# Kernel tuning notes

Hardware: AMD Instinct MI355X
Metric: run time of the kernel (lower is better)

The kernel has to match this reference:

```python
import jax, jax.numpy as jnp
import numpy as np

H = 12  # num_heads (ViT-B)


def setup_inputs() -> dict:
    key = jax.random.key(0)
    ks = jax.random.split(key, 16)
    B, N, C = 128, 197, 768
    eff, hd = H // 2, C // H
    d = {
        'x':  jax.random.normal(ks[0], (B, N, C), jnp.float32),
        'Wq': jax.random.normal(ks[1], (C, C), jnp.float32) * 0.02,
        'bq': jax.random.normal(ks[2], (C,), jnp.float32) * 0.02,
        'Wk': jax.random.normal(ks[3], (C, C), jnp.float32) * 0.02,
        'bk': jax.random.normal(ks[4], (C,), jnp.float32) * 0.02,
        'Wv': jax.random.normal(ks[5], (C, C), jnp.float32) * 0.02,
        'bv': jax.random.normal(ks[6], (C,), jnp.float32) * 0.02,
        'Wp': jax.random.normal(ks[7], (C, C), jnp.float32) * 0.02,
        'bp': jax.random.normal(ks[8], (C,), jnp.float32) * 0.02,
        'lq1': jax.random.normal(ks[9],  (eff, 1, hd), jnp.float32) * 0.02,
        'lk1': jax.random.normal(ks[10], (eff, 1, hd), jnp.float32) * 0.02,
        'lq2': jax.random.normal(ks[11], (eff, 1, hd), jnp.float32) * 0.02,
        'lk2': jax.random.normal(ks[12], (eff, 1, hd), jnp.float32) * 0.02,
        'num_heads': 12,
        'lambda_init': jnp.float32(0.8),
    }
    return d


def reference(x, Wq, bq, Wk, bk, Wv, bv, Wp, bp, lq1, lk1, lq2, lk2, num_heads, lambda_init):
    B, N, C = x.shape
    hd = C // num_heads
    scale = hd ** -0.5

    def heads(y):  # [B,N,C] -> [B,H,N,hd]
        return y.reshape(B, N, num_heads, hd).transpose(0, 2, 1, 3)

    q = heads(x @ Wq.T + bq)
    k = heads(x @ Wk.T + bk)
    v = heads(x @ Wv.T + bv)
    eff = num_heads // 2
    q1, q2 = q[:, :eff], q[:, eff:]
    k1, k2 = k[:, :eff], k[:, eff:]
    v1, v2 = v[:, :eff], v[:, eff:]

    l1 = jnp.exp(jnp.minimum((lq1 * lk1).sum((-1, -2)), 5.0))  # [eff]
    l2 = jnp.exp(jnp.minimum((lq2 * lk2).sum((-1, -2)), 5.0))
    lv = (l1 - l2 + lambda_init).mean()  # scalar

    def attn(qh, kh, vh):  # [B,eff,N,hd]
        s = jnp.einsum('bhnd,bhmd->bhnm', qh, kh) * scale
        a = jax.nn.softmax(s, axis=-1)
        o = jnp.einsum('bhnm,bhmd->bhnd', a, vh)
        return o.transpose(0, 2, 1, 3).reshape(B, N, C // 2)

    x1 = attn(q1, k1, v1)
    x2 = attn(q2, k2, v2)
    out = jnp.concatenate([x1 - lv * x2, x2], axis=-1)
    return out @ Wp.T + bp
```

## Files before the change

### kernel.cpp

```cpp
#include <hip/hip_runtime.h>
#include <hip/hip_bf16.h>
#include <stdint.h>


typedef __attribute__((ext_vector_type(4))) float f32x4;
typedef __attribute__((ext_vector_type(8))) short s16x8;
typedef __attribute__((ext_vector_type(8))) __bf16 bf16x8;

typedef const __attribute__((address_space(1))) void* gptr_t;
typedef __attribute__((address_space(3))) void* lptr_t;

__device__ __forceinline__ f32x4 mfma16(s16x8 a, s16x8 b, f32x4 c) {
  return __builtin_amdgcn_mfma_f32_16x16x32_bf16(
      __builtin_bit_cast(bf16x8, a), __builtin_bit_cast(bf16x8, b), c, 0, 0, 0);
}

__device__ __forceinline__ short f2bf(float f) {
  unsigned u = __float_as_uint(f);
  u += 0x7fffu + ((u >> 16) & 1u);
  return (short)(u >> 16);
}
__device__ __forceinline__ float bf2f(short s) {
  return __uint_as_float(((unsigned)(unsigned short)s) << 16);
}

__device__ __forceinline__ void gload_lds16(const void* g, void* l) {
  __builtin_amdgcn_global_load_lds((gptr_t)g, (lptr_t)l, 16, 0, 0);
}

__global__ void cvt_f32_to_bf16(const float* __restrict__ src,
                                short* __restrict__ dst, long n8) {
  long i = (long)blockIdx.x * blockDim.x + threadIdx.x;
  const long stride = (long)gridDim.x * blockDim.x;
  for (; i < n8; i += stride) {
    const float4 a = ((const float4*)src)[2 * i];
    const float4 b = ((const float4*)src)[2 * i + 1];
    s16x8 o;
    o[0] = f2bf(a.x); o[1] = f2bf(a.y); o[2] = f2bf(a.z); o[3] = f2bf(a.w);
    o[4] = f2bf(b.x); o[5] = f2bf(b.y); o[6] = f2bf(b.z); o[7] = f2bf(b.w);
    ((s16x8*)dst)[i] = o;
  }
}

__global__ void lv_kernel(const float* __restrict__ lq1, const float* __restrict__ lk1,
                          const float* __restrict__ lq2, const float* __restrict__ lk2,
                          const float* __restrict__ lambda_init, float* __restrict__ out) {
  const int l = threadIdx.x;
  float v = 0.f;
  if (l < 6) {
    float d1 = 0.f, d2 = 0.f;
    for (int j = 0; j < 64; ++j) {
      d1 += lq1[l * 64 + j] * lk1[l * 64 + j];
      d2 += lq2[l * 64 + j] * lk2[l * 64 + j];
    }
    v = expf(fminf(d1, 5.f)) - expf(fminf(d2, 5.f));
  }
  v += __shfl_xor(v, 1, 64);
  v += __shfl_xor(v, 2, 64);
  v += __shfl_xor(v, 4, 64);
  if (l == 0) out[0] = v * (1.f / 6.f) + lambda_init[0];
}

__global__ void cvt_wp_prime(const float* __restrict__ Wp,
                             const float* __restrict__ lvp,
                             short* __restrict__ dst) {
  const int idx = blockIdx.x * blockDim.x + threadIdx.x;
  if (idx >= 73728) return;
  const float lv = *lvp;
  const int ic = idx % 96;
  const float4 a = ((const float4*)Wp)[2 * idx];
  const float4 b = ((const float4*)Wp)[2 * idx + 1];
  float v[8] = {a.x, a.y, a.z, a.w, b.x, b.y, b.z, b.w};
  if (ic >= 48) {
    const float4 a2 = ((const float4*)Wp)[2 * idx - 96];
    const float4 b2 = ((const float4*)Wp)[2 * idx - 95];
    v[0] -= lv * a2.x; v[1] -= lv * a2.y; v[2] -= lv * a2.z; v[3] -= lv * a2.w;
    v[4] -= lv * b2.x; v[5] -= lv * b2.y; v[6] -= lv * b2.z; v[7] -= lv * b2.w;
  }
  s16x8 o;
#pragma unroll
  for (int j = 0; j < 8; ++j) o[j] = f2bf(v[j]);
  ((s16x8*)dst)[idx] = o;
}

template <int OUT_BF16>
__global__ __launch_bounds__(256) void gemm_bt(const short* __restrict__ A, int lda,
                                               const short* __restrict__ B,
                                               const float* __restrict__ bias,
                                               void* __restrict__ C,
                                               int M, int N, int K) {
  const int nbx = N >> 7;
  const int nwg = gridDim.x;
  const int qq = nwg >> 3, rr = nwg & 7;
  const int xcd = blockIdx.x & 7, pos = blockIdx.x >> 3;
  const int wg = (xcd < rr ? xcd * (qq + 1) : rr * (qq + 1) + (xcd - rr) * qq) + pos;
  const int bx = wg % nbx;
  const int by = wg / nbx;
  const long m0 = (long)by << 7;
  const int n0 = bx << 7;
  __shared__ short Asm[128 * 64];
  __shared__ short Bsm[128 * 64];
  const int tid = threadIdx.x;
  const int lane = tid & 63;
  const int w = tid >> 6;
  const int wr = w >> 1, wc = w & 1;
  const int r16 = lane & 15, g = lane >> 4;
  f32x4 acc[4][4];
#pragma unroll
  for (int i = 0; i < 4; ++i)
#pragma unroll
    for (int j = 0; j < 4; ++j) acc[i][j] = f32x4{0.f, 0.f, 0.f, 0.f};

  const int nkt = K >> 6;
  for (int kt = 0; kt < nkt; ++kt) {
    __syncthreads();
#pragma unroll
    for (int i = 0; i < 4; ++i) {
      const int c = i * 256 + tid;
      const int row = c >> 3;
      const int lc = (c & 7) ^ (row & 7);
      gload_lds16(A + (m0 + row) * lda + (long)kt * 64 + lc * 8,
                  Asm + i * 2048 + w * 512);
      gload_lds16(B + (long)(n0 + row) * K + (long)kt * 64 + lc * 8,
                  Bsm + i * 2048 + w * 512);
    }
    asm volatile("s_waitcnt vmcnt(0)" ::: "memory");
    __syncthreads();
#pragma unroll
    for (int kk = 0; kk < 2; ++kk) {
      s16x8 av[4], bvv[4];
#pragma unroll
      for (int f = 0; f < 4; ++f) {
        const int ar = wr * 64 + f * 16 + r16;
        av[f] = *(const s16x8*)(Asm + ar * 64 + ((((kk << 2) + g) ^ (ar & 7)) << 3));
        const int br = wc * 64 + f * 16 + r16;
        bvv[f] = *(const s16x8*)(Bsm + br * 64 + ((((kk << 2) + g) ^ (br & 7)) << 3));
      }
#pragma unroll
      for (int fm = 0; fm < 4; ++fm)
#pragma unroll
        for (int fn = 0; fn < 4; ++fn)
          acc[fm][fn] = mfma16(av[fm], bvv[fn], acc[fm][fn]);
    }
  }
#pragma unroll
  for (int fm = 0; fm < 4; ++fm)
#pragma unroll
    for (int fn = 0; fn < 4; ++fn) {
      const int col = n0 + wc * 64 + fn * 16 + r16;
      const float bb = bias[col];
#pragma unroll
      for (int r = 0; r < 4; ++r) {
        const long row = m0 + wr * 64 + fm * 16 + g * 4 + r;
        const float v = acc[fm][fn][r] + bb;
        if (OUT_BF16) ((short*)C)[row * (long)N + col] = f2bf(v);
        else          ((float*)C)[row * (long)N + col] = v;
      }
    }
}

__global__ __launch_bounds__(512, 4) void attn_kernel(short* QKV) {
  const int b = blockIdx.x / 12;
  const int h = blockIdx.x % 12;
  __shared__ short Ksm[208 * 72];
  __shared__ short Vsm[64 * 232];
  __shared__ short Psm[8][2][512];
  const int tid = threadIdx.x;
  const long base = (long)b * 197 * 2304;

  for (int c = tid; c < 208 * 8; c += 512) {
    const int key = c >> 3, dch = c & 7;
    s16x8 val = {};
    if (key < 197)
      val = *(const s16x8*)(QKV + base + (long)key * 2304 + 768 + h * 64 + dch * 8);
    *(s16x8*)(Ksm + key * 72 + dch * 8) = val;
  }
  for (int c = tid; c < 224 * 8; c += 512) {
    const int key = c % 224, dch = c / 224;
    s16x8 val = {};
    if (key < 197)
      val = *(const s16x8*)(QKV + base + (long)key * 2304 + 1536 + h * 64 + dch * 8);
#pragma unroll
    for (int j = 0; j < 8; ++j) Vsm[(dch * 8 + j) * 232 + key] = val[j];
  }
  __syncthreads();

  const int lane = tid & 63, w = tid >> 6;
  const int r16 = lane & 15, g = lane >> 4;
  char* psw = (char*)Psm[w];

  for (int qt = w; qt < 13; qt += 8) {
    const int q0 = qt * 16;
    int qr = q0 + r16;
    if (qr > 196) qr = 196;
    const s16x8 qf0 = *(const s16x8*)(QKV + base + (long)qr * 2304 + h * 64 + g * 8);
    const s16x8 qf1 = *(const s16x8*)(QKV + base + (long)qr * 2304 + h * 64 + 32 + g * 8);

    f32x4 s[13];
#pragma unroll
    for (int kt = 0; kt < 13; ++kt) s[kt] = f32x4{0.f, 0.f, 0.f, 0.f};
#pragma unroll
    for (int kt = 0; kt < 13; ++kt) {
      const int krow = kt * 16 + r16;
      const s16x8 kf0 = *(const s16x8*)(Ksm + krow * 72 + g * 8);
      const s16x8 kf1 = *(const s16x8*)(Ksm + krow * 72 + 32 + g * 8);
      s[kt] = mfma16(qf0, kf0, s[kt]);
      s[kt] = mfma16(qf1, kf1, s[kt]);
    }
    float mr[4] = {-1e30f, -1e30f, -1e30f, -1e30f};
#pragma unroll
    for (int kt = 0; kt < 13; ++kt)
#pragma unroll
      for (int r = 0; r < 4; ++r) {
        float sv = s[kt][r] * 0.125f;
        if (kt == 12 && r16 >= 5) sv = -1e30f;
        s[kt][r] = sv;
        mr[r] = fmaxf(mr[r], sv);
      }
#pragma unroll
    for (int r = 0; r < 4; ++r) {
      mr[r] = fmaxf(mr[r], __shfl_xor(mr[r], 1, 64));
      mr[r] = fmaxf(mr[r], __shfl_xor(mr[r], 2, 64));
      mr[r] = fmaxf(mr[r], __shfl_xor(mr[r], 4, 64));
      mr[r] = fmaxf(mr[r], __shfl_xor(mr[r], 8, 64));
    }
    float sum[4] = {0.f, 0.f, 0.f, 0.f};
#pragma unroll
    for (int kt = 0; kt < 13; ++kt)
#pragma unroll
      for (int r = 0; r < 4; ++r) {
        const float p = __expf(s[kt][r] - mr[r]);
        s[kt][r] = p;
        sum[r] += p;
      }
#pragma unroll
    for (int r = 0; r < 4; ++r) {
      sum[r] += __shfl_xor(sum[r], 1, 64);
      sum[r] += __shfl_xor(sum[r], 2, 64);
      sum[r] += __shfl_xor(sum[r], 4, 64);
      sum[r] += __shfl_xor(sum[r], 8, 64);
    }
    f32x4 o[4];
#pragma unroll
    for (int df = 0; df < 4; ++df) o[df] = f32x4{0.f, 0.f, 0.f, 0.f};
#pragma unroll
    for (int r = 0; r < 4; ++r) {
      const int prow = g * 4 + r;
      const int sw = (prow & 7) << 4;
      *(short*)(psw + ((prow * 64 + r16 * 2) ^ sw)) = f2bf(s[0][r]);
      *(short*)(psw + ((prow * 64 + (r16 + 16) * 2) ^ sw)) = f2bf(s[1][r]);
    }
#pragma unroll
    for (int kb = 0; kb < 7; ++kb) {
      char* bufr = psw + ((kb & 1) << 10);
      char* bufw = psw + (((kb & 1) ^ 1) << 10);
      const s16x8 pa =
          *(const s16x8*)(bufr + ((r16 * 64 + g * 16) ^ ((r16 & 7) << 4)));
      if (kb < 6) {
#pragma unroll
        for (int r = 0; r < 4; ++r) {
          const int prow = g * 4 + r;
          const int sw = (prow & 7) << 4;
          const float p0f = s[2 * kb + 2][r];
          const float p1f = (kb < 5) ? s[2 * kb + 3][r] : 0.f;
          *(short*)(bufw + ((prow * 64 + r16 * 2) ^ sw)) = f2bf(p0f);
          *(short*)(bufw + ((prow * 64 + (r16 + 16) * 2) ^ sw)) = f2bf(p1f);
        }
      }
#pragma unroll
      for (int df = 0; df < 4; ++df) {
        const s16x8 vf = *(const s16x8*)(Vsm + (df * 16 + r16) * 232 + kb * 32 + g * 8);
        o[df] = mfma16(pa, vf, o[df]);
      }
    }
    float rinv[4];
#pragma unroll
    for (int r = 0; r < 4; ++r) rinv[r] = 1.f / sum[r];
#pragma unroll
    for (int df = 0; df < 4; ++df)
#pragma unroll
      for (int r = 0; r < 4; ++r) {
        const int qrow = q0 + g * 4 + r;
        if (qrow < 197)
          QKV[base + (long)qrow * 2304 + h * 64 + df * 16 + r16] =
              f2bf(o[df][r] * rinv[r]);
      }
  }
}

extern "C" void kernel_launch(void* const* d_in, const int* in_sizes, int n_in,
                              void* d_out, int out_size, void* d_ws, size_t ws_size,
                              hipStream_t stream) {
  (void)in_sizes; (void)n_in; (void)out_size; (void)ws_size;
  const float* x   = (const float*)d_in[0];
  const float* Wq  = (const float*)d_in[1];
  const float* bq  = (const float*)d_in[2];
  const float* Wk  = (const float*)d_in[3];
  const float* bk  = (const float*)d_in[4];
  const float* Wv  = (const float*)d_in[5];
  const float* bv  = (const float*)d_in[6];
  const float* Wp  = (const float*)d_in[7];
  const float* bp  = (const float*)d_in[8];
  const float* lq1 = (const float*)d_in[9];
  const float* lk1 = (const float*)d_in[10];
  const float* lq2 = (const float*)d_in[11];
  const float* lk2 = (const float*)d_in[12];
  const float* lambda_init = (const float*)d_in[14];

  char* ws = (char*)d_ws;
  short* xb   = (short*)ws;
  short* wqkv = (short*)(ws + 38731776);
  short* wpb  = (short*)(ws + 42270720);
  float* bqkv = (float*)(ws + 43450368);
  float* lvp  = (float*)(ws + 43459584);
  short* qkv  = (short*)(ws + 43459840);

  cvt_f32_to_bf16<<<2048, 256, 0, stream>>>(x, xb, 19365888 / 8);
  cvt_f32_to_bf16<<<288, 256, 0, stream>>>(Wq, wqkv, 73728);
  cvt_f32_to_bf16<<<288, 256, 0, stream>>>(Wk, wqkv + 589824, 73728);
  cvt_f32_to_bf16<<<288, 256, 0, stream>>>(Wv, wqkv + 1179648, 73728);
  lv_kernel<<<1, 64, 0, stream>>>(lq1, lk1, lq2, lk2, lambda_init, lvp);
  cvt_wp_prime<<<288, 256, 0, stream>>>(Wp, lvp, wpb);
  hipMemcpyAsync(bqkv,        bq, 768 * 4, hipMemcpyDeviceToDevice, stream);
  hipMemcpyAsync(bqkv + 768,  bk, 768 * 4, hipMemcpyDeviceToDevice, stream);
  hipMemcpyAsync(bqkv + 1536, bv, 768 * 4, hipMemcpyDeviceToDevice, stream);

  gemm_bt<1><<<197 * 18, 256, 0, stream>>>(xb, 768, wqkv, bqkv, qkv, 25216, 2304, 768);
  attn_kernel<<<128 * 12, 512, 0, stream>>>(qkv);
  gemm_bt<0><<<197 * 6, 256, 0, stream>>>(qkv, 2304, wpb, bp, d_out, 25216, 768, 768);
}
```

Baseline: 262.5 us.

## Specialize GEMM K at compile time and use one wave per query tile in attention

The GEMM now takes the K tile count as a template parameter, fully unrolls the K loop and precomputes per-thread global load base pointers outside the loop, cutting address arithmetic. The attention kernel launches 1024 threads (16 waves) so each of the 13 query tiles gets its own wave instead of some waves handling two tiles, which removes the tail imbalance. The larger block raises register pressure per workgroup and leaves three idle waves, and the launch-bounds change may limit occupancy.

Measured after the change: 242.4 us. 1.08x faster.

```diff
diff --git a/kernel.cpp b/kernel.cpp
--- a/kernel.cpp
+++ b/kernel.cpp
@@ -83,12 +83,13 @@
   ((s16x8*)dst)[idx] = o;
 }
 
-template <int OUT_BF16>
+template <int OUT_BF16, int NKT>
 __global__ __launch_bounds__(256) void gemm_bt(const short* __restrict__ A, int lda,
                                                const short* __restrict__ B,
                                                const float* __restrict__ bias,
                                                void* __restrict__ C,
-                                               int M, int N, int K) {
+                                               int M, int N) {
+  const int K = NKT * 64;
   const int nbx = N >> 7;
   const int nwg = gridDim.x;
   const int qq = nwg >> 3, rr = nwg & 7;
@@ -105,24 +106,31 @@
   const int w = tid >> 6;
   const int wr = w >> 1, wc = w & 1;
   const int r16 = lane & 15, g = lane >> 4;
+
+  const short* abase[4];
+  const short* bbase[4];
+#pragma unroll
+  for (int i = 0; i < 4; ++i) {
+    const int c = i * 256 + tid;
+    const int row = c >> 3;
+    const int lc = (c & 7) ^ (row & 7);
+    abase[i] = A + (m0 + row) * (long)lda + lc * 8;
+    bbase[i] = B + (long)(n0 + row) * (long)K + lc * 8;
+  }
+
   f32x4 acc[4][4];
 #pragma unroll
   for (int i = 0; i < 4; ++i)
 #pragma unroll
     for (int j = 0; j < 4; ++j) acc[i][j] = f32x4{0.f, 0.f, 0.f, 0.f};
 
-  const int nkt = K >> 6;
-  for (int kt = 0; kt < nkt; ++kt) {
+#pragma unroll
+  for (int kt = 0; kt < NKT; ++kt) {
     __syncthreads();
 #pragma unroll
     for (int i = 0; i < 4; ++i) {
-      const int c = i * 256 + tid;
-      const int row = c >> 3;
-      const int lc = (c & 7) ^ (row & 7);
-      gload_lds16(A + (m0 + row) * lda + (long)kt * 64 + lc * 8,
-                  Asm + i * 2048 + w * 512);
-      gload_lds16(B + (long)(n0 + row) * K + (long)kt * 64 + lc * 8,
-                  Bsm + i * 2048 + w * 512);
+      gload_lds16(abase[i] + kt * 64, Asm + i * 2048 + w * 512);
+      gload_lds16(bbase[i] + kt * 64, Bsm + i * 2048 + w * 512);
     }
     asm volatile("s_waitcnt vmcnt(0)" ::: "memory");
     __syncthreads();
@@ -159,23 +167,23 @@
     }
 }
 
-__global__ __launch_bounds__(512, 4) void attn_kernel(short* QKV) {
+__global__ __launch_bounds__(1024, 4) void attn_kernel(short* QKV) {
   const int b = blockIdx.x / 12;
   const int h = blockIdx.x % 12;
   __shared__ short Ksm[208 * 72];
   __shared__ short Vsm[64 * 232];
-  __shared__ short Psm[8][2][512];
+  __shared__ short Psm[16][2][512];
   const int tid = threadIdx.x;
   const long base = (long)b * 197 * 2304;
 
-  for (int c = tid; c < 208 * 8; c += 512) {
+  for (int c = tid; c < 208 * 8; c += 1024) {
     const int key = c >> 3, dch = c & 7;
     s16x8 val = {};
     if (key < 197)
       val = *(const s16x8*)(QKV + base + (long)key * 2304 + 768 + h * 64 + dch * 8);
     *(s16x8*)(Ksm + key * 72 + dch * 8) = val;
   }
-  for (int c = tid; c < 224 * 8; c += 512) {
+  for (int c = tid; c < 224 * 8; c += 1024) {
     const int key = c % 224, dch = c / 224;
     s16x8 val = {};
     if (key < 197)
@@ -189,8 +197,8 @@
   const int r16 = lane & 15, g = lane >> 4;
   char* psw = (char*)Psm[w];
 
-  for (int qt = w; qt < 13; qt += 8) {
-    const int q0 = qt * 16;
+  if (w < 13) {
+    const int q0 = w * 16;
     int qr = q0 + r16;
     if (qr > 196) qr = 196;
     const s16x8 qf0 = *(const s16x8*)(QKV + base + (long)qr * 2304 + h * 64 + g * 8);
@@ -325,7 +333,9 @@
   hipMemcpyAsync(bqkv + 768,  bk, 768 * 4, hipMemcpyDeviceToDevice, stream);
   hipMemcpyAsync(bqkv + 1536, bv, 768 * 4, hipMemcpyDeviceToDevice, stream);
 
-  gemm_bt<1><<<197 * 18, 256, 0, stream>>>(xb, 768, wqkv, bqkv, qkv, 25216, 2304, 768);
-  attn_kernel<<<128 * 12, 512, 0, stream>>>(qkv);
-  gemm_bt<0><<<197 * 6, 256, 0, stream>>>(qkv, 2304, wpb, bp, d_out, 25216, 768, 768);
-}
+  gemm_bt<1, 12><<<197 * 18, 256, 0, stream>>>(xb, 768, wqkv, bqkv, qkv,
+                                               25216, 2304);
+  attn_kernel<<<128 * 12, 1024, 0, stream>>>(qkv);
+  gemm_bt<0, 12><<<197 * 6, 256, 0, stream>>>(qkv, 2304, wpb, bp, d_out,
+                                              25216, 768);
+}
```
